# Performance work log

Hardware: AMD Instinct MI355X
Metric: run time of the kernel (lower is better)

The kernel has to match this reference:

```python
import jax, jax.numpy as jnp
import numpy as np

N_NODES = 30000
N_EDGES = 300000
N_GRAPHS = 512
SEQ = 1000
HEADS = 10
CH = 78


def setup_inputs() -> dict:
    key = jax.random.key(0)
    ks = jax.random.split(key, 20)
    def w(k, shape, scale=0.02):
        return jax.random.normal(k, shape, jnp.float32) * scale
    x = jax.random.normal(ks[0], (N_NODES, CH), jnp.float32)
    edge_index = jax.random.randint(ks[1], (2, N_EDGES), 0, N_NODES, jnp.int32)
    # every graph gets a contiguous block of nodes (sorted batch vector)
    batch = (jnp.arange(N_NODES) * N_GRAPHS // N_NODES).astype(jnp.int32)
    target = jax.random.randint(ks[2], (N_GRAPHS, SEQ), 0, 26, jnp.int32)
    return {
        "x": x, "edge_index": edge_index, "batch": batch, "target": target,
        "W_gat": w(ks[3], (CH, HEADS * CH)),
        "att_src": w(ks[4], (HEADS, CH), 0.1),
        "att_dst": w(ks[5], (HEADS, CH), 0.1),
        "b_gat": jnp.zeros((HEADS * CH,), jnp.float32),
        "W_gcn": w(ks[6], (HEADS * CH, HEADS * CH)),
        "b_gcn": jnp.zeros((HEADS * CH,), jnp.float32),
        "W_fcg1": w(ks[7], (2 * HEADS * CH, 1500)), "b_fcg1": jnp.zeros((1500,), jnp.float32),
        "W_fcg2": w(ks[8], (1500, 128)), "b_fcg2": jnp.zeros((128,), jnp.float32),
        "emb": w(ks[9], (26, 128), 1.0),
        "W_conv": w(ks[10], (32, 1000, 8)), "b_conv": jnp.zeros((32,), jnp.float32),
        "W_fcxt": w(ks[11], (32 * 121, 128)), "b_fcxt": jnp.zeros((128,), jnp.float32),
        "W_fc1": w(ks[12], (256, 1024)), "b_fc1": jnp.zeros((1024,), jnp.float32),
        "W_fc2": w(ks[13], (1024, 512)), "b_fc2": jnp.zeros((512,), jnp.float32),
        "W_out": w(ks[14], (512, 1)), "b_out": jnp.zeros((1,), jnp.float32),
    }


def reference(x, edge_index, batch, target,
              W_gat, att_src, att_dst, b_gat, W_gcn, b_gcn,
              W_fcg1, b_fcg1, W_fcg2, b_fcg2, emb, W_conv, b_conv,
              W_fcxt, b_fcxt, W_fc1, b_fc1, W_fc2, b_fc2, W_out, b_out):
    N = x.shape[0]
    loop = jnp.arange(N, dtype=edge_index.dtype)
    src = jnp.concatenate([edge_index[0], loop])  # self-loops (PyG default)
    dst = jnp.concatenate([edge_index[1], loop])

    # ---- GATConv(78 -> 78, heads=10, concat) ----
    h = (x @ W_gat).reshape(N, HEADS, CH)           # [N,H,C]
    a_s = jnp.einsum('nhc,hc->nh', h, att_src)      # [N,H]
    a_d = jnp.einsum('nhc,hc->nh', h, att_dst)
    logits = jax.nn.leaky_relu(a_s[src] + a_d[dst], 0.2)   # [E',H]
    m = jax.ops.segment_max(logits, dst, num_segments=N)
    e = jnp.exp(logits - m[dst])
    denom = jax.ops.segment_sum(e, dst, num_segments=N)
    alpha = e / (denom[dst] + 1e-16)                # per-dst softmax
    xg = jax.ops.segment_sum(h[src] * alpha[:, :, None], dst, num_segments=N)
    xg = jax.nn.relu(xg.reshape(N, HEADS * CH) + b_gat)

    # ---- GCNConv(780 -> 780), symmetric norm with self-loops ----
    deg = jax.ops.segment_sum(jnp.ones_like(dst, dtype=xg.dtype), dst, num_segments=N)
    dinv = jax.lax.rsqrt(jnp.maximum(deg, 1.0))
    norm = dinv[src] * dinv[dst]                    # [E']
    xw = xg @ W_gcn
    xg = jax.ops.segment_sum(xw[src] * norm[:, None], dst, num_segments=N) + b_gcn
    xg = jax.nn.relu(xg)

    # ---- global max + mean pooling per graph ----
    gmax = jax.ops.segment_max(xg, batch, num_segments=N_GRAPHS)
    cnt = jax.ops.segment_sum(jnp.ones((N,), xg.dtype), batch, num_segments=N_GRAPHS)
    gmean = jax.ops.segment_sum(xg, batch, num_segments=N_GRAPHS) / cnt[:, None]
    xp = jnp.concatenate([gmax, gmean], axis=1)     # [G,1560]
    xp = jax.nn.relu(xp @ W_fcg1 + b_fcg1)          # dropout = identity (eval)
    xp = xp @ W_fcg2 + b_fcg2                       # [G,128]

    # ---- protein branch ----
    xt = emb[target]                                # [G,1000,128]
    conv = jax.lax.conv_general_dilated(
        xt, W_conv, window_strides=(1,), padding='VALID',
        dimension_numbers=('NCH', 'OIH', 'NCH'))    # [G,32,121]
    conv = conv + b_conv[None, :, None]
    xt = conv.reshape(conv.shape[0], -1) @ W_fcxt + b_fcxt  # [G,128]

    # ---- joint MLP ----
    xc = jnp.concatenate([xp, xt], axis=1)          # [G,256]
    xc = jax.nn.relu(xc @ W_fc1 + b_fc1)
    xc = jax.nn.relu(xc @ W_fc2 + b_fc2)
    return xc @ W_out + b_out                       # [G,1]
```

## Files before the change

kernel.cpp:

```cpp
#include <hip/hip_runtime.h>
#include <hip/hip_bf16.h>
#include <cstdint>
#include <cstddef>

#define N_NODES 30000
#define E0      300000
#define EPRIME  330000
#define NG      512
#define SEQL    1000
#define HEADS   10
#define CHN     78
#define HC      780
#define HP      800
#define MAXD    64

typedef __attribute__((ext_vector_type(8))) short bf16x8;
typedef __attribute__((ext_vector_type(4))) float f32x4;
typedef __attribute__((ext_vector_type(8))) unsigned short u16x8;

static __device__ __forceinline__ int src_of(const int* ei, int e){
  return (e < E0) ? ei[e] : (e - E0);
}
static __device__ __forceinline__ int dst_of(const int* ei, int e){
  return (e < E0) ? ei[E0 + e] : (e - E0);
}
static __device__ __forceinline__ unsigned short f2bf(float f){
  union { float f; unsigned u; } a; a.f = f;
  unsigned r = a.u + 0x7fff + ((a.u >> 16) & 1);
  return (unsigned short)(r >> 16);
}
static __device__ __forceinline__ float bf2f(unsigned short u){
  union { unsigned u; float f; } a; a.u = ((unsigned)u) << 16; return a.f;
}
static __device__ __forceinline__ void gl_lds16(const unsigned short* g, unsigned short* l){
  __builtin_amdgcn_global_load_lds(
      (const __attribute__((address_space(1))) void*)g,
      (__attribute__((address_space(3))) void*)l,
      16, 0, 0);
}

__global__ void k_bucket(const int* __restrict__ ei, int* __restrict__ cnt, int* __restrict__ bkt){
  int e = blockIdx.x*256 + threadIdx.x;
  if (e < EPRIME){
    int d = dst_of(ei, e);
    int s = src_of(ei, e);
    int slot = atomicAdd(&cnt[d], 1);
    if (slot < MAXD) bkt[d*MAXD + slot] = s;
  }
}

static __device__ void transp_tile(const float* __restrict__ src, unsigned short* __restrict__ dst,
                                   int K, int N, int Kp, int bx, int by){
  __shared__ float t[32][33];
  int k0 = bx*32, n0 = by*32;
  int c = threadIdx.x & 31, r = threadIdx.x >> 5;
  #pragma unroll
  for (int i=0;i<4;i++){
    int k = k0 + r + i*8;
    float v = 0.f;
    if (k < K && n0 + c < N) v = src[(size_t)k*N + n0 + c];
    t[r + i*8][c] = v;
  }
  __syncthreads();
  #pragma unroll
  for (int i=0;i<4;i++){
    int nn = n0 + r + i*8;
    int kk = k0 + c;
    if (nn < N && kk < Kp) dst[(size_t)nn*Kp + kk] = f2bf(t[c][r + i*8]);
  }
}

__global__ __launch_bounds__(256) void k_prep(
    const float* __restrict__ x, unsigned short* __restrict__ xb,
    const float* __restrict__ W_gat, unsigned short* __restrict__ wgat_t,
    const float* __restrict__ W_gcn, unsigned short* __restrict__ wgcn_t,
    const float* __restrict__ W_fcg1, unsigned short* __restrict__ wfcg1_t,
    const float* __restrict__ W_conv, float* __restrict__ w2t,
    unsigned short* __restrict__ hbp, unsigned short* __restrict__ xwbp,
    float* __restrict__ xc, float* __restrict__ t1, float* __restrict__ t2, float* __restrict__ fg1,
    const float* __restrict__ b_fcg2, const float* __restrict__ b_fcxt,
    const float* __restrict__ b_fc1, const float* __restrict__ b_fc2,
    const float* __restrict__ b_fcg1, int* __restrict__ cnt)
{
  int b = blockIdx.x;
  int tid = threadIdx.x;
  if (b < 11250){
    int idx = b*256 + tid;
    if (idx < N_NODES*96){
      int n = idx/96, k = idx - n*96;
      xb[idx] = (k < CHN) ? f2bf(x[(size_t)n*CHN + k]) : 0;
    }
    return;
  }
  b -= 11250;
  if (b < 75){ transp_tile(W_gat, wgat_t, CHN, HC, 96, b%3, b/3); return; }
  b -= 75;
  if (b < 625){ transp_tile(W_gcn, wgcn_t, HC, HC, HP, b%25, b/25); return; }
  b -= 625;
  if (b < 2303){ transp_tile(W_fcg1, wfcg1_t, 1560, 1500, 1568, b%49, b/49); return; }
  b -= 2303;
  if (b < 512){
    int g = b;
    int zi = g*256 + tid;
    if (zi < N_NODES) cnt[zi] = 0;
    if (tid < 128){
      xc[(size_t)g*256 + tid]       = b_fcg2[tid];
      xc[(size_t)g*256 + 128 + tid] = b_fcxt[tid];
    }
    for (int i = tid; i < 1024; i += 256) t1[(size_t)g*1024 + i] = b_fc1[i];
    for (int i = tid; i < 512;  i += 256) t2[(size_t)g*512  + i] = b_fc2[i];
    for (int i = tid; i < 1500; i += 256) fg1[(size_t)g*1500 + i] = b_fcg1[i];
    for (int i = tid; i < 59; i += 256){
      int n = g + i*512;
      if (n < N_NODES){
        *reinterpret_cast<unsigned long long*>(hbp  + (size_t)n*HP + HC) = 0ull;
        *reinterpret_cast<unsigned long long*>(xwbp + (size_t)n*HP + HC) = 0ull;
      }
    }
    return;
  }
  b -= 512;
  {
    int o = tid >> 3, k = tid & 7;
    w2t[(size_t)b*256 + tid] = W_conv[(size_t)o*8000 + b*8 + k];
  }
}

__global__ __launch_bounds__(256) void k_mfma_bt(
    const unsigned short* __restrict__ A, const unsigned short* __restrict__ Bt,
    const float* __restrict__ bias, float* __restrict__ C, unsigned short* __restrict__ Cb,
    int M, int N, int Kp, int ldc, int relu,
    int ntc, int ntr, int ntk, int Kc, int accum)
{
  const int total = ntc*ntr*ntk;
  const int per = (total + 7) >> 3;
  const int b = blockIdx.x;
  const int w = (b & 7)*per + (b >> 3);
  if (w >= total) return;
  const int kt = w / (ntc*ntr);
  const int r2 = w - kt*(ntc*ntr);
  const int row_t = r2 / ntc, col_t = r2 - row_t*ntc;
  const int row0 = row_t*128, col0 = col_t*128;
  const int kbeg = kt*Kc;
  const int kend = min(kbeg + Kc, Kp);

  __shared__ unsigned short As[128*32];
  __shared__ unsigned short Bs[128*32];
  const int tid = threadIdx.x;
  const int lane = tid & 63;
  const int wv = tid >> 6;
  const int wm = wv >> 1, wn = wv & 1;
  const int quad = lane >> 4, l16 = lane & 15;
  const int srow = lane >> 2;
  const int scol = (lane & 3) * 8;

  f32x4 acc[4][4];
  #pragma unroll
  for (int mi=0;mi<4;mi++)
    #pragma unroll
    for (int ni=0;ni<4;ni++){
      acc[mi][ni][0]=0.f; acc[mi][ni][1]=0.f; acc[mi][ni][2]=0.f; acc[mi][ni][3]=0.f;
    }

  for (int k0 = kbeg; k0 < kend; k0 += 32){
    #pragma unroll
    for (int i=0;i<2;i++){
      int ch = wv*2 + i;
      int r  = ch*16 + srow;
      gl_lds16(A  + (size_t)(row0 + r)*Kp + k0 + scol, &As[ch*512]);
      gl_lds16(Bt + (size_t)(col0 + r)*Kp + k0 + scol, &Bs[ch*512]);
    }
    __syncthreads();
    bf16x8 af[4], bfr[4];
    #pragma unroll
    for (int mi=0;mi<4;mi++) af[mi]  = *(const bf16x8*)(&As[(wm*64 + mi*16 + l16)*32 + quad*8]);
    #pragma unroll
    for (int ni=0;ni<4;ni++) bfr[ni] = *(const bf16x8*)(&Bs[(wn*64 + ni*16 + l16)*32 + quad*8]);
    #pragma unroll
    for (int mi=0;mi<4;mi++)
      #pragma unroll
      for (int ni=0;ni<4;ni++)
        acc[mi][ni] = __builtin_amdgcn_mfma_f32_16x16x32_bf16(af[mi], bfr[ni], acc[mi][ni], 0,0,0);
    __syncthreads();
  }

  #pragma unroll
  for (int mi=0;mi<4;mi++){
    #pragma unroll
    for (int rr=0;rr<4;rr++){
      int row = row0 + wm*64 + mi*16 + quad*4 + rr;
      if (row >= M) continue;
      #pragma unroll
      for (int ni=0;ni<4;ni++){
        int col = col0 + wn*64 + ni*16 + l16;
        if (col >= N) continue;
        float v = acc[mi][ni][rr];
        if (accum){
          atomicAdd(&C[(size_t)row*ldc + col], v);
        } else {
          if (bias) v += bias[col];
          if (relu) v = fmaxf(v, 0.f);
          if (Cb) Cb[(size_t)row*ldc + col] = f2bf(v);
          else    C [(size_t)row*ldc + col] = v;
        }
      }
    }
  }
}

__global__ __launch_bounds__(256) void k_gemm_sk(const float* __restrict__ A, const float* __restrict__ B,
    float* __restrict__ C, int M, int N, int K, int lda, int ldb, int ldc, int Kc, int relu_a)
{
  __shared__ float As[16][34];
  __shared__ float Bs[16][64];
  const int tid = threadIdx.x;
  const int tx = tid & 15, ty = tid >> 4;
  const int row0 = blockIdx.y * 32, col0 = blockIdx.x * 64;
  const int kbeg = blockIdx.z * Kc;
  const int kend = min(kbeg + Kc, K);
  float acc[2][4];
  #pragma unroll
  for (int i=0;i<2;i++)
    #pragma unroll
    for (int j=0;j<4;j++) acc[i][j] = 0.f;

  for (int k0 = kbeg; k0 < kend; k0 += 16){
    #pragma unroll
    for (int i=0;i<2;i++){
      int idx = tid + i*256;
      int r = idx >> 4, c = idx & 15;
      int gr = row0 + r, gc = k0 + c;
      float v = (gr < M && gc < kend) ? A[(size_t)gr*lda + gc] : 0.f;
      if (relu_a) v = fmaxf(v, 0.f);
      As[c][r] = v;
    }
    #pragma unroll
    for (int i=0;i<4;i++){
      int idx = tid + i*256;
      int r = idx >> 6, c = idx & 63;
      int gr = k0 + r, gc = col0 + c;
      Bs[r][c] = (gr < kend && gc < N) ? B[(size_t)gr*ldb + gc] : 0.f;
    }
    __syncthreads();
    #pragma unroll
    for (int kk=0; kk<16; kk++){
      float a0 = As[kk][ty*2], a1 = As[kk][ty*2+1];
      float b0 = Bs[kk][tx*4], b1 = Bs[kk][tx*4+1], b2 = Bs[kk][tx*4+2], b3 = Bs[kk][tx*4+3];
      acc[0][0]+=a0*b0; acc[0][1]+=a0*b1; acc[0][2]+=a0*b2; acc[0][3]+=a0*b3;
      acc[1][0]+=a1*b0; acc[1][1]+=a1*b1; acc[1][2]+=a1*b2; acc[1][3]+=a1*b3;
    }
    __syncthreads();
  }
  #pragma unroll
  for (int i=0;i<2;i++){
    int r = row0 + ty*2 + i;
    if (r >= M) continue;
    #pragma unroll
    for (int j=0;j<4;j++){
      int c = col0 + tx*4 + j;
      if (c < N) atomicAdd(&C[(size_t)r*ldc + c], acc[i][j]);
    }
  }
}

__global__ __launch_bounds__(256) void k_attn(const unsigned short* __restrict__ hb,
    const float* __restrict__ att_src, const float* __restrict__ att_dst,
    float* __restrict__ a_s, float* __restrict__ a_d){
  __shared__ float ssrc[HC], sdst[HC];
  for (int i = threadIdx.x; i < HC; i += 256){ ssrc[i]=att_src[i]; sdst[i]=att_dst[i]; }
  __syncthreads();
  int idx = blockIdx.x*256 + threadIdx.x;
  if (idx >= N_NODES*HEADS) return;
  int n  = idx / HEADS;
  int hh = idx - n*HEADS;
  const unsigned* hp2 = (const unsigned*)(hb + (size_t)n*HP + hh*CHN);
  const float* as_ = ssrc + hh*CHN;
  const float* ad_ = sdst + hh*CHN;
  float s1=0.f, s2=0.f;
  #pragma unroll 13
  for (int c2=0;c2<39;c2++){
    unsigned u = hp2[c2];
    float v0 = bf2f((unsigned short)(u & 0xffffu));
    float v1 = bf2f((unsigned short)(u >> 16));
    int c = 2*c2;
    s1 += v0*as_[c] + v1*as_[c+1];
    s2 += v0*ad_[c] + v1*ad_[c+1];
  }
  a_s[idx]=s1; a_d[idx]=s2;
}

__global__ __launch_bounds__(256) void k_gat_agg(
    const unsigned short* __restrict__ hb, const float* __restrict__ a_s, const float* __restrict__ a_d,
    const float* __restrict__ b_gat, const int* __restrict__ cnt, const int* __restrict__ bkt,
    unsigned short* __restrict__ xgb, float* __restrict__ dinv)
{
  int half = threadIdx.x >> 7;
  int lt   = threadIdx.x & 127;
  int n = blockIdx.x*2 + half;
  int deg = cnt[n];
  int degc = min(deg, MAXD);
  __shared__ int   s_src[2][MAXD];
  __shared__ float s_adn[2][HEADS];
  __shared__ float s_lg[2][MAXD*HEADS];
  __shared__ float s_al[2][MAXD*HEADS];
  if (lt < HEADS) s_adn[half][lt] = a_d[(size_t)n*HEADS + lt];
  if (lt < degc)  s_src[half][lt] = bkt[n*MAXD + lt];
  __syncthreads();
  for (int idx = lt; idx < degc*HEADS; idx += 128){
    int j = idx/HEADS, t = idx - j*HEADS;
    float l = a_s[(size_t)s_src[half][j]*HEADS + t] + s_adn[half][t];
    s_lg[half][idx] = (l > 0.f) ? l : 0.2f*l;
  }
  __syncthreads();
  if (lt < HEADS){
    float m = -3.4e38f;
    for (int j=0;j<degc;j++) m = fmaxf(m, s_lg[half][j*HEADS+lt]);
    float s = 0.f;
    for (int j=0;j<degc;j++){ float e = __expf(s_lg[half][j*HEADS+lt]-m); s_al[half][j*HEADS+lt]=e; s+=e; }
    float inv = 1.f/(s + 1e-16f);
    for (int j=0;j<degc;j++) s_al[half][j*HEADS+lt] *= inv;
  }
  __syncthreads();
  if (lt < 98){
    int ch0 = lt*8;
    int hlo = min(ch0/CHN, HEADS-1);
    int hhi = min((ch0+7)/CHN, HEADS-1);
    int m   = hhi*CHN - ch0;
    const float* al = &s_al[half][0];
    float acc[8];
    #pragma unroll
    for (int e=0;e<8;e++) acc[e]=0.f;
    auto edge = [&](int j){
      int s = s_src[half][j];
      uint4 v = *((const uint4*)(hb + (size_t)s*HP) + lt);
      float alo = al[j*HEADS + hlo];
      float ahi = al[j*HEADS + hhi];
      unsigned uu[4] = {v.x, v.y, v.z, v.w};
      #pragma unroll
      for (int e2=0;e2<4;e2++){
        float v0 = bf2f((unsigned short)(uu[e2] & 0xffffu));
        float v1 = bf2f((unsigned short)(uu[e2] >> 16));
        float a0 = (2*e2   < m) ? alo : ahi;
        float a1 = (2*e2+1 < m) ? alo : ahi;
        acc[2*e2]   += a0*v0;
        acc[2*e2+1] += a1*v1;
      }
    };
    int j = 0;
    for (; j+2 <= degc; j += 2){ edge(j); edge(j+1); }
    for (; j < degc; ++j) edge(j);
    u16x8 o;
    #pragma unroll
    for (int e=0;e<8;e++){
      int ch = ch0+e;
      float bv = (ch < HC) ? b_gat[ch] : 0.f;
      float ov = (ch < HC) ? fmaxf(acc[e]+bv, 0.f) : 0.f;
      o[e] = f2bf(ov);
    }
    *((u16x8*)(xgb + (size_t)n*HP) + lt) = o;
  } else if (lt < 100){
    u16x8 z = {0,0,0,0,0,0,0,0};
    *((u16x8*)(xgb + (size_t)n*HP) + lt) = z;
  }
  if (lt == 0) dinv[n] = rsqrtf((float)deg);
}

__global__ __launch_bounds__(256) void k_gcn_agg(
    const unsigned short* __restrict__ xwb, const float* __restrict__ dinv, const float* __restrict__ b_gcn,
    const int* __restrict__ cnt, const int* __restrict__ bkt,
    unsigned short* __restrict__ xg2b)
{
  int half = threadIdx.x >> 7;
  int lt   = threadIdx.x & 127;
  int n = blockIdx.x*2 + half;
  int deg = min(cnt[n], MAXD);
  __shared__ int   s_src[2][MAXD];
  __shared__ float s_w[2][MAXD];
  if (lt < deg){
    int s = bkt[n*MAXD + lt];
    s_src[half][lt] = s;
    s_w[half][lt] = dinv[s];
  }
  __syncthreads();
  if (lt < 98){
    int ch0 = lt*8;
    float acc[8];
    #pragma unroll
    for (int e=0;e<8;e++) acc[e]=0.f;
    auto edge = [&](int j){
      int s = s_src[half][j];
      float w = s_w[half][j];
      uint4 v = *((const uint4*)(xwb + (size_t)s*HP) + lt);
      unsigned uu[4] = {v.x, v.y, v.z, v.w};
      #pragma unroll
      for (int e2=0;e2<4;e2++){
        acc[2*e2]   += w*bf2f((unsigned short)(uu[e2] & 0xffffu));
        acc[2*e2+1] += w*bf2f((unsigned short)(uu[e2] >> 16));
      }
    };
    int j = 0;
    for (; j+2 <= deg; j += 2){ edge(j); edge(j+1); }
    for (; j < deg; ++j) edge(j);
    float dn = dinv[n];
    ushort4 o0, o1;
    float r0 = fmaxf(dn*acc[0] + ((ch0   < HC) ? b_gcn[ch0  ] : 0.f), 0.f);
    float r1 = fmaxf(dn*acc[1] + ((ch0+1 < HC) ? b_gcn[ch0+1] : 0.f), 0.f);
    float r2 = fmaxf(dn*acc[2] + ((ch0+2 < HC) ? b_gcn[ch0+2] : 0.f), 0.f);
    float r3 = fmaxf(dn*acc[3] + ((ch0+3 < HC) ? b_gcn[ch0+3] : 0.f), 0.f);
    float r4 = fmaxf(dn*acc[4] + ((ch0+4 < HC) ? b_gcn[ch0+4] : 0.f), 0.f);
    float r5 = fmaxf(dn*acc[5] + ((ch0+5 < HC) ? b_gcn[ch0+5] : 0.f), 0.f);
    float r6 = fmaxf(dn*acc[6] + ((ch0+6 < HC) ? b_gcn[ch0+6] : 0.f), 0.f);
    float r7 = fmaxf(dn*acc[7] + ((ch0+7 < HC) ? b_gcn[ch0+7] : 0.f), 0.f);
    o0.x=f2bf(r0); o0.y=f2bf(r1); o0.z=f2bf(r2); o0.w=f2bf(r3);
    o1.x=f2bf(r4); o1.y=f2bf(r5); o1.z=f2bf(r6); o1.w=f2bf(r7);
    unsigned short* row = xg2b + (size_t)n*HC;
    *(ushort4*)(row + ch0) = o0;
    if (ch0+4 < HC) *(ushort4*)(row + ch0+4) = o1;
  }
}

__global__ __launch_bounds__(256) void k_pool(const unsigned short* __restrict__ xg2b,
                                              unsigned short* __restrict__ xpb){
  int g = blockIdx.x;
  int n0 = (N_NODES*g + NG-1) >> 9;
  int n1 = (N_NODES*(g+1) + NG-1) >> 9;
  float inv = 1.f/(float)(n1 - n0);
  int c4 = threadIdx.x;
  if (c4 < 195){
    const ushort4* x4 = (const ushort4*)xg2b;
    float m0=-3.4e38f,m1=-3.4e38f,m2=-3.4e38f,m3=-3.4e38f;
    float s0=0.f,s1=0.f,s2=0.f,s3=0.f;
    for (int n = n0; n < n1; n++){
      ushort4 v = x4[(size_t)n*195 + c4];
      float a=bf2f(v.x), b=bf2f(v.y), c=bf2f(v.z), d=bf2f(v.w);
      m0=fmaxf(m0,a); m1=fmaxf(m1,b); m2=fmaxf(m2,c); m3=fmaxf(m3,d);
      s0+=a; s1+=b; s2+=c; s3+=d;
    }
    int ch = 4*c4;
    unsigned short* row = xpb + (size_t)g*1568;
    row[ch]=f2bf(m0); row[ch+1]=f2bf(m1); row[ch+2]=f2bf(m2); row[ch+3]=f2bf(m3);
    row[HC+ch]=f2bf(s0*inv); row[HC+ch+1]=f2bf(s1*inv);
    row[HC+ch+2]=f2bf(s2*inv); row[HC+ch+3]=f2bf(s3*inv);
  }
  if (threadIdx.x < 8) xpb[(size_t)g*1568 + 1560 + threadIdx.x] = 0;
}

__global__ __launch_bounds__(256) void k_conv(const int* __restrict__ target,
                                              const float* __restrict__ W2t,
                                              const float* __restrict__ emb, const float* __restrict__ b_conv,
                                              float* __restrict__ convf){
  int g = blockIdx.x;
  int tid = threadIdx.x;
  int o = tid >> 3;
  __shared__ int   tgt[SEQL];
  __shared__ int   cntv[26];
  __shared__ int   startv[27];
  __shared__ int   ofs[26];
  __shared__ alignas(16) unsigned short posv[SEQL];
  __shared__ float U[256*26];
  __shared__ float sE[26*128 + 32];

  for (int i = tid; i < 26*128; i += 256) sE[i] = emb[i];
  if (tid < 32) sE[26*128 + tid] = 0.f;
  if (tid < 26) cntv[tid] = 0;
  const int* tg = target + g*SEQL;
  for (int i = tid; i < SEQL; i += 256) tgt[i] = tg[i];
  __syncthreads();

  for (int i = tid; i < SEQL; i += 256) atomicAdd(&cntv[tgt[i]], 1);
  __syncthreads();
  if (tid == 0){
    int s = 0;
    #pragma unroll
    for (int v = 0; v < 26; v++){ startv[v] = s; ofs[v] = s; s += cntv[v]; }
    startv[26] = s;
  }
  __syncthreads();
  for (int i = tid; i < SEQL; i += 256){
    int v = tgt[i];
    int slot = atomicAdd(&ofs[v], 1);
    posv[slot] = (unsigned short)((v << 10) | i);
  }
  __syncthreads();

  {
    const float* wp2 = W2t + tid;
    float s = 0.f;
    int cur = 0;
    for (int j = 0; j < SEQL; j += 8){
      u16x8 p8 = *(const u16x8*)&posv[j];
      float w[8];
      #pragma unroll
      for (int q = 0; q < 8; q++) w[q] = wp2[((int)p8[q] & 1023) << 8];
      #pragma unroll
      for (int q = 0; q < 8; q++){
        int ve = (int)p8[q] >> 10;
        if (ve != cur){
          U[tid*26 + cur] = s;
          for (int z = cur+1; z < ve; z++) U[tid*26 + z] = 0.f;
          cur = ve; s = 0.f;
        }
        s += w[q];
      }
    }
    U[tid*26 + cur] = s;
    for (int z = cur+1; z < 26; z++) U[tid*26 + z] = 0.f;
  }
  __syncthreads();

  int pg = tid & 7;
  int p0 = pg * 16;
  int np = 121 - p0; if (np > 16) np = 16;
  float acc[16];
  #pragma unroll
  for (int i=0;i<16;i++) acc[i]=0.f;
  for (int v = 0; v < 26; v++){
    float u[8];
    #pragma unroll
    for (int kk=0;kk<8;kk++) u[kk] = U[(o*8 + kk)*26 + v];
    const float* ep = &sE[v*128 + p0];
    float e[24];
    #pragma unroll
    for (int i=0;i<24;i+=4){
      float4 q = *(const float4*)(ep + i);
      e[i]=q.x; e[i+1]=q.y; e[i+2]=q.z; e[i+3]=q.w;
    }
    #pragma unroll
    for (int pl=0; pl<16; pl++){
      acc[pl] += u[0]*e[pl]   + u[1]*e[pl+1] + u[2]*e[pl+2] + u[3]*e[pl+3]
               + u[4]*e[pl+4] + u[5]*e[pl+5] + u[6]*e[pl+6] + u[7]*e[pl+7];
    }
  }
  float bo = b_conv[o];
  for (int pl=0; pl<np; pl++)
    convf[(size_t)g*3872 + o*121 + p0 + pl] = acc[pl] + bo;
}

__global__ __launch_bounds__(64) void k_final(const float* __restrict__ t2, const float* __restrict__ W_out,
                                              const float* __restrict__ b_out, float* __restrict__ out){
  int g = blockIdx.x;
  int lane = threadIdx.x;
  const float* r = t2 + (size_t)g*512;
  float s = 0.f;
  #pragma unroll
  for (int i = lane; i < 512; i += 64) s += fmaxf(r[i], 0.f)*W_out[i];
  #pragma unroll
  for (int off=32; off; off>>=1) s += __shfl_down(s, off);
  if (lane==0) out[g] = s + b_out[0];
}

extern "C" void kernel_launch(void* const* d_in, const int* in_sizes, int n_in,
                              void* d_out, int out_size, void* d_ws, size_t ws_size,
                              hipStream_t stream) {
  const float* x      = (const float*)d_in[0];
  const int*   ei     = (const int*)  d_in[1];
  const int*   target = (const int*)  d_in[3];
  const float* W_gat  = (const float*)d_in[4];
  const float* att_src= (const float*)d_in[5];
  const float* att_dst= (const float*)d_in[6];
  const float* b_gat  = (const float*)d_in[7];
  const float* W_gcn  = (const float*)d_in[8];
  const float* b_gcn  = (const float*)d_in[9];
  const float* W_fcg1 = (const float*)d_in[10];
  const float* b_fcg1 = (const float*)d_in[11];
  const float* W_fcg2 = (const float*)d_in[12];
  const float* b_fcg2 = (const float*)d_in[13];
  const float* emb    = (const float*)d_in[14];
  const float* W_conv = (const float*)d_in[15];
  const float* b_conv = (const float*)d_in[16];
  const float* W_fcxt = (const float*)d_in[17];
  const float* b_fcxt = (const float*)d_in[18];
  const float* W_fc1  = (const float*)d_in[19];
  const float* b_fc1  = (const float*)d_in[20];
  const float* W_fc2  = (const float*)d_in[21];
  const float* b_fc2  = (const float*)d_in[22];
  const float* W_out  = (const float*)d_in[23];
  const float* b_out  = (const float*)d_in[24];
  float* out = (float*)d_out;

  char* ws = (char*)d_ws;
  size_t off = 0;
  auto alloc = [&](size_t bytes)->char*{
    char* p = ws + off;
    off += (bytes + 255) & ~(size_t)255;
    return p;
  };
  unsigned short* hb  = (unsigned short*)alloc((size_t)N_NODES*HP*2);
  unsigned short* xwb = (unsigned short*)alloc((size_t)N_NODES*HP*2);
  unsigned short* xu  = (unsigned short*)alloc((size_t)N_NODES*HP*2);
  unsigned short* xb     = (unsigned short*)alloc((size_t)N_NODES*96*2);
  unsigned short* wgat_t = (unsigned short*)alloc((size_t)HC*96*2);
  unsigned short* wgcn_t = (unsigned short*)alloc((size_t)HC*HP*2);
  unsigned short* wfcg1_t= (unsigned short*)alloc((size_t)1500*1568*2);
  unsigned short* xpb    = (unsigned short*)alloc((size_t)NG*1568*2);
  float* a_s    = (float*)alloc((size_t)N_NODES*HEADS*4);
  float* a_d    = (float*)alloc((size_t)N_NODES*HEADS*4);
  float* dinv   = (float*)alloc((size_t)N_NODES*4);
  int*   cnt    = (int*)  alloc((size_t)N_NODES*4);
  int*   bkt    = (int*)  alloc((size_t)N_NODES*MAXD*4);
  float* fg1    = (float*)alloc((size_t)NG*1500*4);
  float* convf  = (float*)alloc((size_t)NG*3872*4);
  float* xc     = (float*)alloc((size_t)NG*256*4);
  float* t1     = (float*)alloc((size_t)NG*1024*4);
  float* t2     = (float*)alloc((size_t)NG*512*4);
  float* w2t    = (float*)alloc((size_t)SEQL*256*4);

  unsigned short* xgb  = xu;
  unsigned short* xg2b = xu;

  k_prep<<<11250+75+625+2303+512+1000, 256, 0, stream>>>(
      x, xb, W_gat, wgat_t, W_gcn, wgcn_t, W_fcg1, wfcg1_t, W_conv, w2t, hb, xwb,
      xc, t1, t2, fg1, b_fcg2, b_fcxt, b_fc1, b_fc2, b_fcg1, cnt);

  k_bucket<<<(EPRIME+255)/256, 256, 0, stream>>>(ei, cnt, bkt);

  auto swgrid = [](int total){ return 8 * ((total + 7) / 8); };

  k_mfma_bt<<<swgrid(7*235), 256, 0, stream>>>(xb, wgat_t, nullptr, nullptr, hb,
                                               N_NODES, HC, 96, HP, 0, 7, 235, 1, 96, 0);
  k_attn<<<(N_NODES*HEADS+255)/256, 256, 0, stream>>>(hb, att_src, att_dst, a_s, a_d);
  k_gat_agg<<<N_NODES/2, 256, 0, stream>>>(hb, a_s, a_d, b_gat, cnt, bkt, xgb, dinv);

  k_mfma_bt<<<swgrid(7*235), 256, 0, stream>>>(xgb, wgcn_t, nullptr, nullptr, xwb,
                                               N_NODES, HC, HP, HP, 0, 7, 235, 1, HP, 0);
  k_gcn_agg<<<N_NODES/2, 256, 0, stream>>>(xwb, dinv, b_gcn, cnt, bkt, xg2b);

  k_pool<<<NG, 256, 0, stream>>>(xg2b, xpb);
  k_mfma_bt<<<swgrid(12*4*2), 256, 0, stream>>>(xpb, wfcg1_t, nullptr, fg1, nullptr,
                                                NG, 1500, 1568, 1500, 0, 12, 4, 2, 800, 1);
  k_gemm_sk<<<dim3(2, 16, 8), 256, 0, stream>>>(fg1, W_fcg2, xc, NG, 128, 1500, 1500, 128, 256, 192, 1);

  k_conv<<<NG, 256, 0, stream>>>(target, w2t, emb, b_conv, convf);
  k_gemm_sk<<<dim3(2, 16, 8), 256, 0, stream>>>(convf, W_fcxt, xc + 128, NG, 128, 3872, 3872, 128, 256, 512, 0);

  k_gemm_sk<<<dim3(16, 16, 1), 256, 0, stream>>>(xc, W_fc1, t1, NG, 1024, 256, 256, 1024, 1024, 256, 0);
  k_gemm_sk<<<dim3(8, 16, 2), 256, 0, stream>>>(t1, W_fc2, t2, NG, 512, 1024, 1024, 512, 512, 512, 1);
  k_final<<<NG, 64, 0, stream>>>(t2, W_out, b_out, out);
}
```

Measured before the change: 824.3 us.

## Pad per-head channels to 80 and fold conv branch into prep kernel

The GAT projection output is stored with each head padded from 78 to 80 channels, and the GCN weight is transposed into the same padded layout. This lets the aggregation kernel use one attention coefficient per 8-channel vector instead of picking between two heads per lane. The protein convolution kernel is merged into the prep kernel as 512 extra blocks, with the W_conv transpose moved to its own earlier launch. The merge removes a separate launch and lets the conv work overlap with the prep work, but the prep kernel now carries the conv's large shared-memory footprint for every block, which may reduce occupancy for the light elementwise blocks.

```diff
diff --git a/kernel.cpp b/kernel.cpp
--- a/kernel.cpp
+++ b/kernel.cpp
@@ -49,8 +49,14 @@
   }
 }
 
+__global__ __launch_bounds__(256) void k_w2t(const float* __restrict__ W_conv, float* __restrict__ w2t){
+  int b = blockIdx.x;
+  int o = threadIdx.x >> 3, k = threadIdx.x & 7;
+  w2t[(size_t)b*256 + threadIdx.x] = W_conv[(size_t)o*8000 + b*8 + k];
+}
+
 static __device__ void transp_tile(const float* __restrict__ src, unsigned short* __restrict__ dst,
-                                   int K, int N, int Kp, int bx, int by){
+                                   int K, int N, int Kp, int bx, int by, int hpad){
   __shared__ float t[32][33];
   int k0 = bx*32, n0 = by*32;
   int c = threadIdx.x & 31, r = threadIdx.x >> 5;
@@ -66,8 +72,102 @@
   for (int i=0;i<4;i++){
     int nn = n0 + r + i*8;
     int kk = k0 + c;
-    if (nn < N && kk < Kp) dst[(size_t)nn*Kp + kk] = f2bf(t[c][r + i*8]);
-  }
+    if (nn < N){
+      if (hpad){
+        if (kk < K){
+          int hh = kk/78;
+          dst[(size_t)nn*Kp + hh*80 + (kk - hh*78)] = f2bf(t[c][r + i*8]);
+        }
+      } else {
+        if (kk < Kp) dst[(size_t)nn*Kp + kk] = f2bf(t[c][r + i*8]);
+      }
+    }
+  }
+}
+
+static __device__ void conv_body(int g, int tid, const int* __restrict__ target,
+                                 const float* __restrict__ W2t, const float* __restrict__ emb,
+                                 const float* __restrict__ b_conv, float* __restrict__ convf){
+  int o = tid >> 3;
+  __shared__ int   tgt[SEQL];
+  __shared__ int   cntv[26];
+  __shared__ int   startv[27];
+  __shared__ int   ofs[26];
+  __shared__ alignas(16) unsigned short posv[SEQL];
+  __shared__ float U[256*26];
+  __shared__ float sE[26*128 + 32];
+
+  for (int i = tid; i < 26*128; i += 256) sE[i] = emb[i];
+  if (tid < 32) sE[26*128 + tid] = 0.f;
+  if (tid < 26) cntv[tid] = 0;
+  const int* tg = target + g*SEQL;
+  for (int i = tid; i < SEQL; i += 256) tgt[i] = tg[i];
+  __syncthreads();
+  for (int i = tid; i < SEQL; i += 256) atomicAdd(&cntv[tgt[i]], 1);
+  __syncthreads();
+  if (tid == 0){
+    int s = 0;
+    #pragma unroll
+    for (int v = 0; v < 26; v++){ startv[v] = s; ofs[v] = s; s += cntv[v]; }
+    startv[26] = s;
+  }
+  __syncthreads();
+  for (int i = tid; i < SEQL; i += 256){
+    int v = tgt[i];
+    int slot = atomicAdd(&ofs[v], 1);
+    posv[slot] = (unsigned short)((v << 10) | i);
+  }
+  __syncthreads();
+  {
+    const float* wp2 = W2t + tid;
+    float s = 0.f;
+    int cur = 0;
+    for (int j = 0; j < SEQL; j += 8){
+      u16x8 p8 = *(const u16x8*)&posv[j];
+      float w[8];
+      #pragma unroll
+      for (int q = 0; q < 8; q++) w[q] = wp2[((int)p8[q] & 1023) << 8];
+      #pragma unroll
+      for (int q = 0; q < 8; q++){
+        int ve = (int)p8[q] >> 10;
+        if (ve != cur){
+          U[tid*26 + cur] = s;
+          for (int z = cur+1; z < ve; z++) U[tid*26 + z] = 0.f;
+          cur = ve; s = 0.f;
+        }
+        s += w[q];
+      }
+    }
+    U[tid*26 + cur] = s;
+    for (int z = cur+1; z < 26; z++) U[tid*26 + z] = 0.f;
+  }
+  __syncthreads();
+  int pg = tid & 7;
+  int p0 = pg * 16;
+  int np = 121 - p0; if (np > 16) np = 16;
+  float acc[16];
+  #pragma unroll
+  for (int i=0;i<16;i++) acc[i]=0.f;
+  for (int v = 0; v < 26; v++){
+    float u[8];
+    #pragma unroll
+    for (int kk=0;kk<8;kk++) u[kk] = U[(o*8 + kk)*26 + v];
+    const float* ep = &sE[v*128 + p0];
+    float e[24];
+    #pragma unroll
+    for (int i=0;i<24;i+=4){
+      float4 q = *(const float4*)(ep + i);
+      e[i]=q.x; e[i+1]=q.y; e[i+2]=q.z; e[i+3]=q.w;
+    }
+    #pragma unroll
+    for (int pl=0; pl<16; pl++){
+      acc[pl] += u[0]*e[pl]   + u[1]*e[pl+1] + u[2]*e[pl+2] + u[3]*e[pl+3]
+               + u[4]*e[pl+4] + u[5]*e[pl+5] + u[6]*e[pl+6] + u[7]*e[pl+7];
+    }
+  }
+  float bo = b_conv[o];
+  for (int pl=0; pl<np; pl++)
+    convf[(size_t)g*3872 + o*121 + p0 + pl] = acc[pl] + bo;
 }
 
 __global__ __launch_bounds__(256) void k_prep(
@@ -75,8 +175,9 @@
     const float* __restrict__ W_gat, unsigned short* __restrict__ wgat_t,
     const float* __restrict__ W_gcn, unsigned short* __restrict__ wgcn_t,
     const float* __restrict__ W_fcg1, unsigned short* __restrict__ wfcg1_t,
-    const float* __restrict__ W_conv, float* __restrict__ w2t,
-    unsigned short* __restrict__ hbp, unsigned short* __restrict__ xwbp,
+    const int* __restrict__ target, const float* __restrict__ w2t,
+    const float* __restrict__ emb, const float* __restrict__ b_conv, float* __restrict__ convf,
+    unsigned short* __restrict__ xwbp,
     float* __restrict__ xc, float* __restrict__ t1, float* __restrict__ t2, float* __restrict__ fg1,
     const float* __restrict__ b_fcg2, const float* __restrict__ b_fcxt,
     const float* __restrict__ b_fc1, const float* __restrict__ b_fc2,
@@ -84,6 +185,8 @@
 {
   int b = blockIdx.x;
   int tid = threadIdx.x;
+  if (b < 512){ conv_body(b, tid, target, w2t, emb, b_conv, convf); return; }
+  b -= 512;
   if (b < 11250){
     int idx = b*256 + tid;
     if (idx < N_NODES*96){
@@ -93,13 +196,13 @@
     return;
   }
   b -= 11250;
-  if (b < 75){ transp_tile(W_gat, wgat_t, CHN, HC, 96, b%3, b/3); return; }
+  if (b < 75){ transp_tile(W_gat, wgat_t, CHN, HC, 96, b%3, b/3, 0); return; }
   b -= 75;
-  if (b < 625){ transp_tile(W_gcn, wgcn_t, HC, HC, HP, b%25, b/25); return; }
+  if (b < 625){ transp_tile(W_gcn, wgcn_t, HC, HC, HP, b%25, b/25, 1); return; }
   b -= 625;
-  if (b < 2303){ transp_tile(W_fcg1, wfcg1_t, 1560, 1500, 1568, b%49, b/49); return; }
+  if (b < 2303){ transp_tile(W_fcg1, wfcg1_t, 1560, 1500, 1568, b%49, b/49, 0); return; }
   b -= 2303;
-  if (b < 512){
+  {
     int g = b;
     int zi = g*256 + tid;
     if (zi < N_NODES) cnt[zi] = 0;
@@ -112,17 +215,13 @@
     for (int i = tid; i < 1500; i += 256) fg1[(size_t)g*1500 + i] = b_fcg1[i];
     for (int i = tid; i < 59; i += 256){
       int n = g + i*512;
-      if (n < N_NODES){
-        *reinterpret_cast<unsigned long long*>(hbp  + (size_t)n*HP + HC) = 0ull;
+      if (n < N_NODES)
         *reinterpret_cast<unsigned long long*>(xwbp + (size_t)n*HP + HC) = 0ull;
-      }
-    }
-    return;
-  }
-  b -= 512;
-  {
-    int o = tid >> 3, k = tid & 7;
-    w2t[(size_t)b*256 + tid] = W_conv[(size_t)o*8000 + b*8 + k];
+    }
+    if (zi < 7800){
+      int nn = zi/10, p = zi - (zi/10)*10;
+      *reinterpret_cast<unsigned*>(wgcn_t + (size_t)nn*HP + p*80 + 78) = 0u;
+    }
   }
 }
 
@@ -130,7 +229,7 @@
     const unsigned short* __restrict__ A, const unsigned short* __restrict__ Bt,
     const float* __restrict__ bias, float* __restrict__ C, unsigned short* __restrict__ Cb,
     int M, int N, int Kp, int ldc, int relu,
-    int ntc, int ntr, int ntk, int Kc, int accum)
+    int ntc, int ntr, int ntk, int Kc, int accum, int hpad)
 {
   const int total = ntc*ntr*ntk;
   const int per = (total + 7) >> 3;
@@ -200,8 +299,10 @@
         } else {
           if (bias) v += bias[col];
           if (relu) v = fmaxf(v, 0.f);
-          if (Cb) Cb[(size_t)row*ldc + col] = f2bf(v);
-          else    C [(size_t)row*ldc + col] = v;
+          int cs = col;
+          if (hpad){ int hh = col/78; cs = hh*80 + (col - hh*78); }
+          if (Cb) Cb[(size_t)row*ldc + cs] = f2bf(v);
+          else    C [(size_t)row*ldc + cs] = v;
         }
       }
     }
@@ -273,7 +374,7 @@
   if (idx >= N_NODES*HEADS) return;
   int n  = idx / HEADS;
   int hh = idx - n*HEADS;
-  const unsigned* hp2 = (const unsigned*)(hb + (size_t)n*HP + hh*CHN);
+  const unsigned* hp2 = (const unsigned*)(hb + (size_t)n*HP + hh*80);
   const float* as_ = ssrc + hh*CHN;
   const float* ad_ = sdst + hh*CHN;
   float s1=0.f, s2=0.f;
@@ -321,29 +422,24 @@
     for (int j=0;j<degc;j++) s_al[half][j*HEADS+lt] *= inv;
   }
   __syncthreads();
-  if (lt < 98){
-    int ch0 = lt*8;
-    int hlo = min(ch0/CHN, HEADS-1);
-    int hhi = min((ch0+7)/CHN, HEADS-1);
-    int m   = hhi*CHN - ch0;
-    const float* al = &s_al[half][0];
+  if (lt < 100){
+    int h = lt/10;
+    int r = lt - h*10;
+    int nv = (r==9) ? 6 : 8;
+    int chb = h*CHN + r*8;
+    const float* alp = &s_al[half][h];
     float acc[8];
     #pragma unroll
     for (int e=0;e<8;e++) acc[e]=0.f;
     auto edge = [&](int j){
       int s = s_src[half][j];
+      float a = alp[j*HEADS];
       uint4 v = *((const uint4*)(hb + (size_t)s*HP) + lt);
-      float alo = al[j*HEADS + hlo];
-      float ahi = al[j*HEADS + hhi];
       unsigned uu[4] = {v.x, v.y, v.z, v.w};
       #pragma unroll
       for (int e2=0;e2<4;e2++){
-        float v0 = bf2f((unsigned short)(uu[e2] & 0xffffu));
-        float v1 = bf2f((unsigned short)(uu[e2] >> 16));
-        float a0 = (2*e2   < m) ? alo : ahi;
-        float a1 = (2*e2+1 < m) ? alo : ahi;
-        acc[2*e2]   += a0*v0;
-        acc[2*e2+1] += a1*v1;
+        acc[2*e2]   += a*bf2f((unsigned short)(uu[e2] & 0xffffu));
+        acc[2*e2+1] += a*bf2f((unsigned short)(uu[e2] >> 16));
       }
     };
     int j = 0;
@@ -352,15 +448,10 @@
     u16x8 o;
     #pragma unroll
     for (int e=0;e<8;e++){
-      int ch = ch0+e;
-      float bv = (ch < HC) ? b_gat[ch] : 0.f;
-      float ov = (ch < HC) ? fmaxf(acc[e]+bv, 0.f) : 0.f;
+      float ov = (e < nv) ? fmaxf(acc[e] + b_gat[chb+e], 0.f) : 0.f;
       o[e] = f2bf(ov);
     }
     *((u16x8*)(xgb + (size_t)n*HP) + lt) = o;
-  } else if (lt < 100){
-    u16x8 z = {0,0,0,0,0,0,0,0};
-    *((u16x8*)(xgb + (size_t)n*HP) + lt) = z;
   }
   if (lt == 0) dinv[n] = rsqrtf((float)deg);
 }
@@ -445,97 +536,6 @@
   if (threadIdx.x < 8) xpb[(size_t)g*1568 + 1560 + threadIdx.x] = 0;
 }
 
-__global__ __launch_bounds__(256) void k_conv(const int* __restrict__ target,
-                                              const float* __restrict__ W2t,
-                                              const float* __restrict__ emb, const float* __restrict__ b_conv,
-                                              float* __restrict__ convf){
-  int g = blockIdx.x;
-  int tid = threadIdx.x;
-  int o = tid >> 3;
-  __shared__ int   tgt[SEQL];
-  __shared__ int   cntv[26];
-  __shared__ int   startv[27];
-  __shared__ int   ofs[26];
-  __shared__ alignas(16) unsigned short posv[SEQL];
-  __shared__ float U[256*26];
-  __shared__ float sE[26*128 + 32];
-
-  for (int i = tid; i < 26*128; i += 256) sE[i] = emb[i];
-  if (tid < 32) sE[26*128 + tid] = 0.f;
-  if (tid < 26) cntv[tid] = 0;
-  const int* tg = target + g*SEQL;
-  for (int i = tid; i < SEQL; i += 256) tgt[i] = tg[i];
-  __syncthreads();
-
-  for (int i = tid; i < SEQL; i += 256) atomicAdd(&cntv[tgt[i]], 1);
-  __syncthreads();
-  if (tid == 0){
-    int s = 0;
-    #pragma unroll
-    for (int v = 0; v < 26; v++){ startv[v] = s; ofs[v] = s; s += cntv[v]; }
-    startv[26] = s;
-  }
-  __syncthreads();
-  for (int i = tid; i < SEQL; i += 256){
-    int v = tgt[i];
-    int slot = atomicAdd(&ofs[v], 1);
-    posv[slot] = (unsigned short)((v << 10) | i);
-  }
-  __syncthreads();
-
-  {
-    const float* wp2 = W2t + tid;
-    float s = 0.f;
-    int cur = 0;
-    for (int j = 0; j < SEQL; j += 8){
-      u16x8 p8 = *(const u16x8*)&posv[j];
-      float w[8];
-      #pragma unroll
-      for (int q = 0; q < 8; q++) w[q] = wp2[((int)p8[q] & 1023) << 8];
-      #pragma unroll
-      for (int q = 0; q < 8; q++){
-        int ve = (int)p8[q] >> 10;
-        if (ve != cur){
-          U[tid*26 + cur] = s;
-          for (int z = cur+1; z < ve; z++) U[tid*26 + z] = 0.f;
-          cur = ve; s = 0.f;
-        }
-        s += w[q];
-      }
-    }
-    U[tid*26 + cur] = s;
-    for (int z = cur+1; z < 26; z++) U[tid*26 + z] = 0.f;
-  }
-  __syncthreads();
-
-  int pg = tid & 7;
-  int p0 = pg * 16;
-  int np = 121 - p0; if (np > 16) np = 16;
-  float acc[16];
-  #pragma unroll
-  for (int i=0;i<16;i++) acc[i]=0.f;
-  for (int v = 0; v < 26; v++){
-    float u[8];
-    #pragma unroll
-    for (int kk=0;kk<8;kk++) u[kk] = U[(o*8 + kk)*26 + v];
-    const float* ep = &sE[v*128 + p0];
-    float e[24];
-    #pragma unroll
-    for (int i=0;i<24;i+=4){
-      float4 q = *(const float4*)(ep + i);
-      e[i]=q.x; e[i+1]=q.y; e[i+2]=q.z; e[i+3]=q.w;
-    }
-    #pragma unroll
-    for (int pl=0; pl<16; pl++){
-      acc[pl] += u[0]*e[pl]   + u[1]*e[pl+1] + u[2]*e[pl+2] + u[3]*e[pl+3]
-               + u[4]*e[pl+4] + u[5]*e[pl+5] + u[6]*e[pl+6] + u[7]*e[pl+7];
-    }
-  }
-  float bo = b_conv[o];
-  for (int pl=0; pl<np; pl++)
-    convf[(size_t)g*3872 + o*121 + p0 + pl] = acc[pl] + bo;
-}
-
 __global__ __launch_bounds__(64) void k_final(const float* __restrict__ t2, const float* __restrict__ W_out,
                                               const float* __restrict__ b_out, float* __restrict__ out){
   int g = blockIdx.x;
@@ -608,8 +608,11 @@
   unsigned short* xgb  = xu;
   unsigned short* xg2b = xu;
 
-  k_prep<<<11250+75+625+2303+512+1000, 256, 0, stream>>>(
-      x, xb, W_gat, wgat_t, W_gcn, wgcn_t, W_fcg1, wfcg1_t, W_conv, w2t, hb, xwb,
+  k_w2t<<<1000, 256, 0, stream>>>(W_conv, w2t);
+
+  k_prep<<<512+11250+75+625+2303+512, 256, 0, stream>>>(
+      x, xb, W_gat, wgat_t, W_gcn, wgcn_t, W_fcg1, wfcg1_t,
+      target, w2t, emb, b_conv, convf, xwb,
       xc, t1, t2, fg1, b_fcg2, b_fcxt, b_fc1, b_fc2, b_fcg1, cnt);
 
   k_bucket<<<(EPRIME+255)/256, 256, 0, stream>>>(ei, cnt, bkt);
@@ -617,20 +620,19 @@
   auto swgrid = [](int total){ return 8 * ((total + 7) / 8); };
 
   k_mfma_bt<<<swgrid(7*235), 256, 0, stream>>>(xb, wgat_t, nullptr, nullptr, hb,
-                                               N_NODES, HC, 96, HP, 0, 7, 235, 1, 96, 0);
+                                               N_NODES, HC, 96, HP, 0, 7, 235, 1, 96, 0, 1);
   k_attn<<<(N_NODES*HEADS+255)/256, 256, 0, stream>>>(hb, att_src, att_dst, a_s, a_d);
   k_gat_agg<<<N_NODES/2, 256, 0, stream>>>(hb, a_s, a_d, b_gat, cnt, bkt, xgb, dinv);
 
   k_mfma_bt<<<swgrid(7*235), 256, 0, stream>>>(xgb, wgcn_t, nullptr, nullptr, xwb,
-                                               N_NODES, HC, HP, HP, 0, 7, 235, 1, HP, 0);
+                                               N_NODES, HC, HP, HP, 0, 7, 235, 1, HP, 0, 0);
   k_gcn_agg<<<N_NODES/2, 256, 0, stream>>>(xwb, dinv, b_gcn, cnt, bkt, xg2b);
 
   k_pool<<<NG, 256, 0, stream>>>(xg2b, xpb);
   k_mfma_bt<<<swgrid(12*4*2), 256, 0, stream>>>(xpb, wfcg1_t, nullptr, fg1, nullptr,
-                                                NG, 1500, 1568, 1500, 0, 12, 4, 2, 800, 1);
+                                                NG, 1500, 1568, 1500, 0, 12, 4, 2, 800, 1, 0);
   k_gemm_sk<<<dim3(2, 16, 8), 256, 0, stream>>>(fg1, W_fcg2, xc, NG, 128, 1500, 1500, 128, 256, 192, 1);
 
-  k_conv<<<NG, 256, 0, stream>>>(target, w2t, emb, b_conv, convf);
   k_gemm_sk<<<dim3(2, 16, 8), 256, 0, stream>>>(convf, W_fcxt, xc + 128, NG, 128, 3872, 3872, 128, 256, 512, 0);
 
   k_gemm_sk<<<dim3(16, 16, 1), 256, 0, stream>>>(xc, W_fc1, t1, NG, 1024, 256, 256, 1024, 1024, 256, 0);
```

New measurement: 825.9 us. About the same (+0.2%).
